# Kernel tuning notes

Hardware: AMD Instinct MI355X
Metric: run time of the kernel (lower is better)

## Reference

```python
import jax, jax.numpy as jnp
from jax import lax
import numpy as np

EPS_COS = 1e-8   # cosine-similarity eps (matches F.cosine_similarity default scale)
EPS_IN = 1e-5    # InstanceNorm2d default eps
NEG = -1e9


def _conv3(x, w, b):
    # x: [B,C,H,W], w: [O,I,3,3]
    y = lax.conv_general_dilated(x, w, (1, 1), 'SAME',
                                 dimension_numbers=('NCHW', 'OIHW', 'NCHW'))
    return y + b[None, :, None, None]


def _inorm(x):
    m = jnp.mean(x, axis=(2, 3), keepdims=True)
    v = jnp.var(x, axis=(2, 3), keepdims=True)
    return (x - m) * lax.rsqrt(v + EPS_IN)


def _shift(former, latter, mask):
    # former/latter: [B,C,H,W]; mask: [H,W] int (1 = hole).
    # For every masked pixel, find the most cosine-similar UNMASKED pixel in the
    # latter (known-region encoder) features and copy the former feature from it.
    B, C, H, W = former.shape
    L = H * W
    lat = lax.stop_gradient(latter).reshape(B, C, L)           # attention is non-differentiable
    latn = lat / (jnp.linalg.norm(lat, axis=1, keepdims=True) + EPS_COS)
    sim = jnp.einsum('bcm,bcn->bmn', latn, latn)               # [B,L,L] query m -> key n
    mflat = mask.reshape(L) > 0
    sim = jnp.where(mflat[None, None, :], NEG, sim)            # keys must be unmasked
    idx = jnp.argmax(sim, axis=-1)                             # [B,L]
    fflat = former.reshape(B, C, L)
    gathered = jnp.take_along_axis(fflat, jnp.broadcast_to(idx[:, None, :], (B, C, L)), axis=2)
    shift = jnp.where(mflat[None, None, :], gathered, 0.0)     # zeros outside the hole
    return shift.reshape(B, C, H, W)


def setup_inputs() -> dict:
    key = jax.random.key(0)
    ks = jax.random.split(key, 6)
    B, C, H, W = 8, 256, 64, 64
    inp = jax.random.normal(ks[0], (B, 2 * C, H, W), dtype=jnp.float32)
    mask = jax.random.randint(ks[1], (H, W), 0, 2, dtype=jnp.int32)
    s1 = 1.0 / float(np.sqrt(2 * C * 9))
    s2 = 1.0 / float(np.sqrt(C * 9))
    W1 = jax.random.uniform(ks[2], (C, 2 * C, 3, 3), jnp.float32, -s1, s1)
    b1 = jax.random.uniform(ks[3], (C,), jnp.float32, -s1, s1)
    W2 = jax.random.uniform(ks[4], (C, C, 3, 3), jnp.float32, -s2, s2)
    b2 = jax.random.uniform(ks[5], (C,), jnp.float32, -s2, s2)
    return {"input": inp, "mask": mask, "W1": W1, "b1": b1, "W2": W2, "b2": b2}


def reference(input, mask, W1, b1, W2, b2):
    C = input.shape[1] // 2
    F_c = input[:, :C]          # former (decoder) features
    F_s = input[:, C:]          # latter (encoder) features
    F_shift = _shift(F_c, F_s, mask)
    F_fuse = F_c * F_shift
    F_com = jnp.concatenate([F_c, F_fuse], axis=1)             # [B,2C,H,W]
    h = jax.nn.relu(_inorm(_conv3(F_com, W1, b1)))
    res = _inorm(_conv3(h, W2, b2))
    return jnp.concatenate([F_c + res, F_s], axis=1)
```

## Files before the change

kernel.cpp:

```cpp
#include <hip/hip_runtime.h>
#include <hip/hip_bf16.h>
#include <math.h>

#define L 4096
#define C 256
#define B 8

typedef __attribute__((ext_vector_type(8))) short bf16x8;
typedef __attribute__((ext_vector_type(8))) ushort u16x8;
typedef __attribute__((ext_vector_type(4))) float f32x4;

__device__ inline ushort f2bu(float f) { __hip_bfloat16 h = __float2bfloat16(f); return *(ushort*)&h; }
__device__ inline float bu2f(ushort u) { __hip_bfloat16 h; *(ushort*)&h = u; return __bfloat162float(h); }

#define SWZ(c) ((((c) >> 1) & 3) << 4)

__global__ __launch_bounds__(256) void compact_mask(
    const int* __restrict__ mask, int* __restrict__ counts,
    int* __restrict__ maskedOrig, int* __restrict__ unmaskOrig,
    int* __restrict__ posOf)
{
    __shared__ int smM[256], smU[256];
    int t = threadIdx.x;
    int flags[16];
    int cm = 0, cu = 0;
    for (int k = 0; k < 16; ++k) {
        int l = t * 16 + k;
        int f = mask[l] > 0;
        flags[k] = f;
        cm += f; cu += !f;
    }
    smM[t] = cm; smU[t] = cu;
    __syncthreads();
    for (int off = 1; off < 256; off <<= 1) {
        int vM = 0, vU = 0;
        if (t >= off) { vM = smM[t - off]; vU = smU[t - off]; }
        __syncthreads();
        smM[t] += vM; smU[t] += vU;
        __syncthreads();
    }
    if (t == 255) { counts[0] = smM[255]; counts[1] = smU[255]; }
    int pm = smM[t] - cm, pu = smU[t] - cu;
    for (int k = 0; k < 16; ++k) {
        int l = t * 16 + k;
        if (flags[k]) { maskedOrig[pm] = l; posOf[l] = pm; pm++; }
        else          { unmaskOrig[pu] = l; posOf[l] = pu; pu++; }
    }
}

__global__ __launch_bounds__(256) void norm_transpose(
    const float* __restrict__ input, const int* __restrict__ mask,
    const int* __restrict__ counts, const int* __restrict__ posOf,
    ushort* __restrict__ fsnh, ushort* __restrict__ fsnl)
{
    int bx = blockIdx.x;
    int b = bx >> 7;
    int l0 = (bx & 127) * 32;
    __shared__ float tile[256 * 33];
    __shared__ float part[8 * 33];
    __shared__ float denom[32];
    __shared__ int   rowdst[32];
    int t = threadIdx.x;
    int lsub = t & 31, cg = t >> 5;
    for (int cc = 0; cc < 256; cc += 8) {
        int c = cc + cg;
        tile[c * 33 + lsub] = input[((size_t)(b * 512 + 256 + c)) * L + l0 + lsub];
    }
    __syncthreads();
    float s = 0.f;
    for (int c = cg; c < 256; c += 8) { float v = tile[c * 33 + lsub]; s = fmaf(v, v, s); }
    part[cg * 33 + lsub] = s;
    __syncthreads();
    if (t < 32) {
        float s2 = 0.f;
        for (int g = 0; g < 8; ++g) s2 += part[g * 33 + t];
        denom[t] = sqrtf(s2) + 1e-8f;
        int l = l0 + t;
        int Nm = counts[0];
        rowdst[t] = (mask[l] > 0) ? posOf[l] : (Nm + posOf[l]);
    }
    __syncthreads();
    for (int ls = 0; ls < 32; ++ls) {
        int r = rowdst[ls];
        float d = denom[ls];
        float val = tile[t * 33 + ls] / d;
        ushort h = f2bu(val);
        float hf = bu2f(h);
        ushort lo = f2bu(val - hf);
        size_t o = ((size_t)b * L + r) * C + t;
        fsnh[o] = h;
        fsnl[o] = lo;
    }
}

__global__ __launch_bounds__(256, 2) void sim_argmax_v6(
    const ushort* __restrict__ hi, const ushort* __restrict__ lo,
    const int* __restrict__ counts,
    float* __restrict__ pval, int* __restrict__ pidx)
{
    __shared__ ushort ldsB[2 * 64 * 256];
    const int Nm = counts[0], Nu = counts[1];
    const int b = blockIdx.z;
    const int m0 = blockIdx.y * 64;
    const int half = blockIdx.x;
    const int t = threadIdx.x;
    const int w = t >> 6, l = t & 63;
    const int lm = l & 15, lk = l >> 4;
    const int key = lm << 4;

    const int nct = (Nu + 63) >> 6;
    const int hs = (nct + 1) >> 1;
    const int cA = half * hs, cB = half ? nct : hs;

    float bestv[4]; int bestn[4];
#pragma unroll
    for (int r = 0; r < 4; ++r) { bestv[r] = -3e38f; bestn[r] = 0; }

    if (m0 < Nm && cA < cB) {
        const char* bytesH = (const char*)hi;
        const char* bytesL = (const char*)lo;
        const size_t bL = (size_t)b * L;
        char* ldsc = (char*)ldsB;

#define STAGE(cc) do { \
    size_t gb = (bL + (size_t)Nm + (size_t)(cc) * 64) * 512; \
    _Pragma("unroll") \
    for (int i = 0; i < 8; ++i) { \
        int j = w * 8 + i; \
        int x = j * 1024 + l * 16; \
        int sx = x ^ (((x >> 9) & 15) << 4); \
        __builtin_amdgcn_global_load_lds((const __attribute__((address_space(1))) unsigned*)(bytesH + gb + sx), \
            (__attribute__((address_space(3))) unsigned*)(ldsc + j * 1024), 16, 0, 0); \
        __builtin_amdgcn_global_load_lds((const __attribute__((address_space(1))) unsigned*)(bytesL + gb + sx), \
            (__attribute__((address_space(3))) unsigned*)(ldsc + 32768 + j * 1024), 16, 0, 0); \
    } \
} while (0)

        STAGE(cA);

        const int rA = m0 + w * 16 + lm;
        bf16x8 ah[8], al[8];
        {
            const ushort* aH = hi + (bL + rA) * C + lk * 8;
            const ushort* aL = lo + (bL + rA) * C + lk * 8;
#pragma unroll
            for (int ks = 0; ks < 8; ++ks) {
                ah[ks] = *(const bf16x8*)(aH + ks * 32);
                al[ks] = *(const bf16x8*)(aL + ks * 32);
            }
        }

        for (int c = cA; c < cB; ++c) {
            asm volatile("s_waitcnt vmcnt(0)" ::: "memory");
            __syncthreads();
            f32x4 acc[4];
#pragma unroll
            for (int nf = 0; nf < 4; ++nf) acc[nf] = (f32x4){0.f, 0.f, 0.f, 0.f};
#pragma unroll
            for (int ks = 0; ks < 8; ++ks) {
                bf16x8 bh[4], bl[4];
#pragma unroll
                for (int nf = 0; nf < 4; ++nf) {
                    int row = nf * 16 + lm;
                    int addr = row * 512 + ((ks * 64 + lk * 16) ^ key);
                    bh[nf] = *(const bf16x8*)(ldsc + addr);
                    bl[nf] = *(const bf16x8*)(ldsc + 32768 + addr);
                }
#pragma unroll
                for (int nf = 0; nf < 4; ++nf)
                    acc[nf] = __builtin_amdgcn_mfma_f32_16x16x32_bf16(ah[ks], bh[nf], acc[nf], 0, 0, 0);
#pragma unroll
                for (int nf = 0; nf < 4; ++nf)
                    acc[nf] = __builtin_amdgcn_mfma_f32_16x16x32_bf16(ah[ks], bl[nf], acc[nf], 0, 0, 0);
#pragma unroll
                for (int nf = 0; nf < 4; ++nf)
                    acc[nf] = __builtin_amdgcn_mfma_f32_16x16x32_bf16(al[ks], bh[nf], acc[nf], 0, 0, 0);
            }
            __syncthreads();
            if (c + 1 < cB) STAGE(c + 1);
            int nbase = c * 64;
#pragma unroll
            for (int r = 0; r < 4; ++r) {
#pragma unroll
                for (int nf = 0; nf < 4; ++nf) {
                    int n = nbase + nf * 16 + lm;
                    float v = acc[nf][r];
                    if (n < Nu && v > bestv[r]) { bestv[r] = v; bestn[r] = n; }
                }
            }
        }
#undef STAGE
    }

    if (m0 >= Nm) return;
#pragma unroll
    for (int r = 0; r < 4; ++r) {
        float bv = bestv[r]; int bn = bestn[r];
#pragma unroll
        for (int mk = 1; mk < 16; mk <<= 1) {
            float ov = __shfl_xor(bv, mk, 64);
            int   on = __shfl_xor(bn, mk, 64);
            if (ov > bv || (ov == bv && on < bn)) { bv = ov; bn = on; }
        }
        if (lm == 0) {
            int m = m0 + w * 16 + lk * 4 + r;
            size_t o = ((size_t)(b * 4096 + m)) * 2 + half;
            pval[o] = bv; pidx[o] = bn;
        }
    }
}

__global__ __launch_bounds__(256) void wprep(
    const float* __restrict__ W1, const float* __restrict__ W2,
    ushort* __restrict__ W1bf, ushort* __restrict__ W2bf)
{
    int gid = blockIdx.x * 256 + threadIdx.x;
    const int N1 = 256 * 512 * 9;
    const int N2 = 256 * 256 * 9;
    if (gid < N1) {
        int ci = gid & 511; int rest = gid >> 9;
        int tau = rest % 9; int co = rest / 9;
        W1bf[gid] = f2bu(W1[((size_t)(co * 512 + ci)) * 9 + tau]);
    } else if (gid < N1 + N2) {
        int g = gid - N1;
        int ci = g & 255; int rest = g >> 8;
        int tau = rest % 9; int co = rest / 9;
        W2bf[g] = f2bu(W2[((size_t)(co * 256 + ci)) * 9 + tau]);
    }
}

__global__ __launch_bounds__(256) void in_prep1(
    const float* __restrict__ input, ushort* __restrict__ inT)
{
    int b = blockIdx.y;
    int p0 = blockIdx.x * 32;
    __shared__ float tile[256][33];
    int t = threadIdx.x;
    int pq = t & 7;
    for (int cc = 0; cc < 256; cc += 32) {
        int ci = cc + (t >> 3);
        float4 v = *(const float4*)(input + ((size_t)(b * 512 + ci)) * L + p0 + pq * 4);
        tile[ci][pq * 4 + 0] = v.x; tile[ci][pq * 4 + 1] = v.y;
        tile[ci][pq * 4 + 2] = v.z; tile[ci][pq * 4 + 3] = v.w;
    }
    __syncthreads();
    int c8 = t & 31;
    for (int pp = 0; pp < 32; pp += 8) {
        int pixloc = pp + (t >> 5);
        u16x8 u;
#pragma unroll
        for (int j = 0; j < 8; ++j) u[j] = f2bu(tile[c8 * 8 + j][pixloc]);
        *(u16x8*)(inT + ((size_t)(b * 4096 + p0 + pixloc)) * 512 + c8 * 8) = u;
    }
}

__global__ __launch_bounds__(256) void in_prep2(
    ushort* __restrict__ inT, const int* __restrict__ mask,
    const float* __restrict__ pval, const int* __restrict__ pidx,
    const int* __restrict__ posOf, const int* __restrict__ unmaskOrig)
{
    int gid = blockIdx.x * 256 + threadIdx.x;
    int c8 = gid & 31;
    int pix = (gid >> 5) & 4095;
    int b = gid >> 17;
    u16x8 out8;
    if (mask[pix] > 0) {
        int m = posOf[pix];
        size_t base = ((size_t)(b * 4096 + m)) * 2;
        float bv = pval[base]; int bn = pidx[base];
        float v1 = pval[base + 1]; int n1 = pidx[base + 1];
        if (v1 > bv || (v1 == bv && n1 < bn)) { bn = n1; }
        int n = unmaskOrig[bn];
        const ushort* rp = inT + ((size_t)(b * 4096 + pix)) * 512 + c8 * 8;
        const ushort* rn = inT + ((size_t)(b * 4096 + n)) * 512 + c8 * 8;
        u16x8 a = *(const u16x8*)rp;
        u16x8 bb = *(const u16x8*)rn;
#pragma unroll
        for (int j = 0; j < 8; ++j) out8[j] = f2bu(bu2f(a[j]) * bu2f(bb[j]));
    } else {
#pragma unroll
        for (int j = 0; j < 8; ++j) out8[j] = 0;
    }
    *(u16x8*)(inT + ((size_t)(b * 4096 + pix)) * 512 + 256 + c8 * 8) = out8;
}

template<int CKROW, int NORM_IN>
__global__ __launch_bounds__(256, 2) void conv_mfma(
    const ushort* __restrict__ Abf, const ushort* __restrict__ Wbf,
    const float* __restrict__ mrsIn,
    ushort* __restrict__ outH, float* __restrict__ psum)
{
    __shared__ float4 ldsv[62208 / 16];
    char* lds = (char*)ldsv;
    char* ldsB = lds + 25344;
    const int t = threadIdx.x;
    const int w = t >> 6;
    const int l = t & 63;
    const int lm = l & 15, lk = l >> 4;
    const int b = blockIdx.z;
    const int y0 = blockIdx.x * 4;
    const int c0 = blockIdx.y * 64;
    const int yw = y0 + w;
    const size_t abase = (size_t)b * 4096 * CKROW;

    f32x4 acc[4][4];
#pragma unroll
    for (int g = 0; g < 4; ++g)
#pragma unroll
        for (int nf = 0; nf < 4; ++nf) acc[g][nf] = (f32x4){0.f, 0.f, 0.f, 0.f};

    if (t < 48) {
        int r = t >> 3;
        int hX = ((t >> 2) & 1) ? 65 : 0;
        int hk = t & 3;
        *(float4*)(lds + (r * 66 + hX) * 64 + ((hk * 16) ^ SWZ(hX))) = (float4){0.f,0.f,0.f,0.f};
    }

    const int NKC = CKROW / 32;
    for (int kc = 0; kc < NKC; ++kc) {
        __syncthreads();
        {
            int x = t >> 2;
            int k8 = t & 3;
            int cX = x + 1;
            char* dbase = lds + cX * 64 + ((k8 * 16) ^ SWZ(cX));
            if (NORM_IN) {
                const float* mb = mrsIn + (size_t)b * 512 + (size_t)(kc * 32 + k8 * 8) * 2;
                float mm[8], rr[8];
#pragma unroll
                for (int j = 0; j < 8; ++j) { mm[j] = mb[2 * j]; rr[j] = mb[2 * j + 1]; }
#pragma unroll
                for (int r = 0; r < 6; ++r) {
                    int yy = y0 - 1 + r;
                    float4 ov = (float4){0.f, 0.f, 0.f, 0.f};
                    if (yy >= 0 && yy < 64) {
                        float4 v = *(const float4*)(Abf + abase + (size_t)(yy * 64 + x) * CKROW + kc * 32 + k8 * 8);
                        u16x8 u = *(u16x8*)&v;
                        u16x8 o;
#pragma unroll
                        for (int j = 0; j < 8; ++j) {
                            float z = (bu2f(u[j]) - mm[j]) * rr[j];
                            o[j] = f2bu(z > 0.f ? z : 0.f);
                        }
                        ov = *(float4*)&o;
                    }
                    *(float4*)(dbase + r * (66 * 64)) = ov;
                }
            } else {
#pragma unroll
                for (int r = 0; r < 6; ++r) {
                    int yy = y0 - 1 + r;
                    float4 v;
                    if (yy >= 0 && yy < 64)
                        v = *(const float4*)(Abf + abase + (size_t)(yy * 64 + x) * CKROW + kc * 32 + k8 * 8);
                    else
                        v = (float4){0.f, 0.f, 0.f, 0.f};
                    *(float4*)(dbase + r * (66 * 64)) = v;
                }
            }
            int cl = t >> 2;
            char* dbaseB = ldsB + cl * 64 + ((k8 * 16) ^ SWZ(cl));
            const ushort* sbase = Wbf + ((size_t)(c0 + cl) * 9) * CKROW + kc * 32 + k8 * 8;
#pragma unroll
            for (int tau = 0; tau < 9; ++tau) {
                *(float4*)(dbaseB + tau * (64 * 64)) = *(const float4*)(sbase + (size_t)tau * CKROW);
            }
        }
        __syncthreads();
#pragma unroll
        for (int ky = 0; ky < 3; ++ky) {
            int r = w + ky;
#pragma unroll
            for (int kx = 0; kx < 3; ++kx) {
                int tau = ky * 3 + kx;
                bf16x8 bfr[4];
#pragma unroll
                for (int nf = 0; nf < 4; ++nf) {
                    int cl = nf * 16 + lm;
                    bfr[nf] = *(bf16x8*)(ldsB + (tau * 64 + cl) * 64 + ((lk * 16) ^ SWZ(cl)));
                }
#pragma unroll
                for (int g = 0; g < 4; ++g) {
                    int aX = g * 16 + lm + kx;
                    bf16x8 afr = *(bf16x8*)(lds + (r * 66 + aX) * 64 + ((lk * 16) ^ SWZ(aX)));
#pragma unroll
                    for (int nf = 0; nf < 4; ++nf)
                        acc[g][nf] = __builtin_amdgcn_mfma_f32_16x16x32_bf16(afr, bfr[nf], acc[g][nf], 0, 0, 0);
                }
            }
        }
    }

#pragma unroll
    for (int g = 0; g < 4; ++g)
#pragma unroll
        for (int nf = 0; nf < 4; ++nf) {
            int cout = c0 + nf * 16 + lm;
#pragma unroll
            for (int r = 0; r < 4; ++r) {
                int pix = yw * 64 + g * 16 + lk * 4 + r;
                outH[((size_t)(b * 4096 + pix)) * 256 + cout] = f2bu(acc[g][nf][r]);
            }
        }

    float s[4], q[4];
#pragma unroll
    for (int nf = 0; nf < 4; ++nf) {
        float ss = 0.f, qq = 0.f;
#pragma unroll
        for (int g = 0; g < 4; ++g)
#pragma unroll
            for (int r = 0; r < 4; ++r) { float v = acc[g][nf][r]; ss += v; qq = fmaf(v, v, qq); }
        ss += __shfl_xor(ss, 16, 64); ss += __shfl_xor(ss, 32, 64);
        qq += __shfl_xor(qq, 16, 64); qq += __shfl_xor(qq, 32, 64);
        s[nf] = ss; q[nf] = qq;
    }
    __syncthreads();
    float* S = (float*)lds;
    float* Q = (float*)(lds + 1024);
    if (l < 16) {
#pragma unroll
        for (int nf = 0; nf < 4; ++nf) {
            S[w * 64 + nf * 16 + l] = s[nf];
            Q[w * 64 + nf * 16 + l] = q[nf];
        }
    }
    __syncthreads();
    if (t < 64) {
        float ts = 0.f, tq = 0.f;
#pragma unroll
        for (int w2 = 0; w2 < 4; ++w2) { ts += S[w2 * 64 + t]; tq += Q[w2 * 64 + t]; }
        size_t o = (((size_t)(b * 256 + c0 + t)) * 16 + blockIdx.x) * 2;
        psum[o] = ts; psum[o + 1] = tq;
    }
}

__global__ __launch_bounds__(256) void stats_reduce(
    const float* __restrict__ psum, float* __restrict__ mrs)
{
    int b = blockIdx.x;
    int c = threadIdx.x;
    float s = 0.f, q = 0.f;
    size_t base = ((size_t)(b * 256 + c)) * 16;
    for (int k = 0; k < 16; ++k) { s += psum[(base + k) * 2]; q += psum[(base + k) * 2 + 1]; }
    float mean = s * (1.f / 4096.f);
    float var = q * (1.f / 4096.f) - mean * mean;
    float rs = rsqrtf(var + 1e-5f);
    mrs[(b * 256 + c) * 2] = mean;
    mrs[(b * 256 + c) * 2 + 1] = rs;
}

__global__ __launch_bounds__(256) void finalize_fs(
    const ushort* __restrict__ resbf, const float* __restrict__ mrs,
    const float* __restrict__ input, float* __restrict__ out)
{
    __shared__ float tileT[256][33];
    int bx = blockIdx.x;
    int t = threadIdx.x;
    if (bx < 8192) {
        size_t i = (size_t)bx * 256 + t;
        size_t b = i >> 18;
        size_t r = i & 262143;
        size_t o = ((size_t)(b * 512 + 256)) * 1024 + r;
        ((float4*)out)[o] = ((const float4*)input)[o];
        return;
    }
    int fb = bx - 8192;
    int b = fb >> 7;
    int p0 = (fb & 127) * 32;
    int c8 = t & 31;
    for (int pp = 0; pp < 32; pp += 8) {
        int pixloc = pp + (t >> 5);
        u16x8 u = *(const u16x8*)(resbf + (((size_t)(b * 4096 + p0 + pixloc)) << 8) + c8 * 8);
#pragma unroll
        for (int j = 0; j < 8; ++j) tileT[c8 * 8 + j][pixloc] = bu2f(u[j]);
    }
    __syncthreads();
    int pq = t & 7;
    for (int cc = 0; cc < 256; cc += 32) {
        int c = cc + (t >> 3);
        float m = mrs[(b * 256 + c) * 2];
        float rs = mrs[(b * 256 + c) * 2 + 1];
        size_t off = ((size_t)(b * 512 + c)) * L + p0 + pq * 4;
        float4 f = *(const float4*)(input + off);
        float4 o;
        o.x = f.x + (tileT[c][pq * 4 + 0] - m) * rs;
        o.y = f.y + (tileT[c][pq * 4 + 1] - m) * rs;
        o.z = f.z + (tileT[c][pq * 4 + 2] - m) * rs;
        o.w = f.w + (tileT[c][pq * 4 + 3] - m) * rs;
        *(float4*)(out + off) = o;
    }
}

extern "C" void kernel_launch(void* const* d_in, const int* in_sizes, int n_in,
                              void* d_out, int out_size, void* d_ws, size_t ws_size,
                              hipStream_t stream) {
    const float* input = (const float*)d_in[0];
    const int*   mask  = (const int*)d_in[1];
    const float* W1    = (const float*)d_in[2];
    const float* W2    = (const float*)d_in[4];
    float* out = (float*)d_out;
    (void)in_sizes; (void)n_in; (void)out_size; (void)ws_size;

    char* ob = (char*)d_out;
    char* wp = (char*)d_ws;

    ushort* fsnh = (ushort*)ob;
    ushort* fsnl = (ushort*)(ob + 16777216);
    float*  pval = (float*)(ob + 33554432);
    int*    pidx = (int*)(ob + 37748736);
    ushort* inT  = (ushort*)ob;
    ushort* hraw = (ushort*)(ob + 33554432);

    ushort* resbf  = (ushort*)wp;
    ushort* W1bf   = (ushort*)(wp + 16777216);
    ushort* W2bf   = (ushort*)(wp + 19136512);
    float*  psum1  = (float*)(wp + 20316160);
    float*  psum2  = (float*)(wp + 20578304);
    float*  mrs1   = (float*)(wp + 20840448);
    float*  mrs2   = (float*)(wp + 20856832);
    int* counts     = (int*)(wp + 20873216);
    int* maskedOrig = counts + 4;
    int* unmaskOrig = maskedOrig + L;
    int* posOf      = unmaskOrig + L;

    compact_mask<<<1, 256, 0, stream>>>(mask, counts, maskedOrig, unmaskOrig, posOf);
    norm_transpose<<<1024, 256, 0, stream>>>(input, mask, counts, posOf, fsnh, fsnl);
    sim_argmax_v6<<<dim3(2, 64, 8), 256, 0, stream>>>(fsnh, fsnl, counts, pval, pidx);
    wprep<<<6912, 256, 0, stream>>>(W1, W2, W1bf, W2bf);
    in_prep1<<<dim3(128, 8), 256, 0, stream>>>(input, inT);
    in_prep2<<<4096, 256, 0, stream>>>(inT, mask, pval, pidx, posOf, unmaskOrig);
    conv_mfma<512, 0><<<dim3(16, 4, 8), 256, 0, stream>>>(inT, W1bf, (const float*)nullptr, hraw, psum1);
    stats_reduce<<<8, 256, 0, stream>>>(psum1, mrs1);
    conv_mfma<256, 1><<<dim3(16, 4, 8), 256, 0, stream>>>(hraw, W2bf, mrs1, resbf, psum2);
    stats_reduce<<<8, 256, 0, stream>>>(psum2, mrs2);
    finalize_fs<<<9216, 256, 0, stream>>>(resbf, mrs2, input, out);
}
```

Baseline: 266.9 us.

## Double-buffer key tiles in sim_argmax with 32-key chunks and async prefetch

The similarity/argmax kernel now stages 32-key chunks into two LDS buffers and prefetches chunk c+2 while computing chunk c. It waits only on the older loads (vmcnt(8)) and uses plain s_barrier instead of a full drain. This is meant to overlap global-to-LDS loads with the MFMA work, which were serialized before. In exchange each chunk does half the MFMAs per barrier, so per-iteration sync and argmax overhead doubles relative to compute.

Result: no change. 270.3 us (+1.3%).

```diff
diff --git a/kernel.cpp b/kernel.cpp
--- a/kernel.cpp
+++ b/kernel.cpp
@@ -93,12 +93,12 @@
     }
 }
 
-__global__ __launch_bounds__(256, 2) void sim_argmax_v6(
+__global__ __launch_bounds__(256, 2) void sim_argmax_v8(
     const ushort* __restrict__ hi, const ushort* __restrict__ lo,
     const int* __restrict__ counts,
     float* __restrict__ pval, int* __restrict__ pidx)
 {
-    __shared__ ushort ldsB[2 * 64 * 256];
+    __shared__ ushort ldsB[32768];
     const int Nm = counts[0], Nu = counts[1];
     const int b = blockIdx.z;
     const int m0 = blockIdx.y * 64;
@@ -108,7 +108,7 @@
     const int lm = l & 15, lk = l >> 4;
     const int key = lm << 4;
 
-    const int nct = (Nu + 63) >> 6;
+    const int nct = (Nu + 31) >> 5;
     const int hs = (nct + 1) >> 1;
     const int cA = half * hs, cB = half ? nct : hs;
 
@@ -122,21 +122,21 @@
         const size_t bL = (size_t)b * L;
         char* ldsc = (char*)ldsB;
 
-#define STAGE(cc) do { \
-    size_t gb = (bL + (size_t)Nm + (size_t)(cc) * 64) * 512; \
+#define STAGE(bofs, cc) do { \
+    size_t gb = (bL + (size_t)Nm + (size_t)(cc) * 32) * 512; \
     _Pragma("unroll") \
-    for (int i = 0; i < 8; ++i) { \
-        int j = w * 8 + i; \
-        int x = j * 1024 + l * 16; \
+    for (int i = 0; i < 4; ++i) { \
+        int x = i * 4096 + t * 16; \
         int sx = x ^ (((x >> 9) & 15) << 4); \
         __builtin_amdgcn_global_load_lds((const __attribute__((address_space(1))) unsigned*)(bytesH + gb + sx), \
-            (__attribute__((address_space(3))) unsigned*)(ldsc + j * 1024), 16, 0, 0); \
+            (__attribute__((address_space(3))) unsigned*)(ldsc + (bofs) + x), 16, 0, 0); \
         __builtin_amdgcn_global_load_lds((const __attribute__((address_space(1))) unsigned*)(bytesL + gb + sx), \
-            (__attribute__((address_space(3))) unsigned*)(ldsc + 32768 + j * 1024), 16, 0, 0); \
+            (__attribute__((address_space(3))) unsigned*)(ldsc + (bofs) + 16384 + x), 16, 0, 0); \
     } \
 } while (0)
 
-        STAGE(cA);
+        STAGE(0, cA);
+        if (cA + 1 < cB) STAGE(32768, cA + 1);
 
         const int rA = m0 + w * 16 + lm;
         bf16x8 ah[8], al[8];
@@ -151,38 +151,40 @@
         }
 
         for (int c = cA; c < cB; ++c) {
-            asm volatile("s_waitcnt vmcnt(0)" ::: "memory");
-            __syncthreads();
-            f32x4 acc[4];
-#pragma unroll
-            for (int nf = 0; nf < 4; ++nf) acc[nf] = (f32x4){0.f, 0.f, 0.f, 0.f};
+            int bob = ((c - cA) & 1) * 32768;
+            if (c + 1 < cB) asm volatile("s_waitcnt vmcnt(8)" ::: "memory");
+            else            asm volatile("s_waitcnt vmcnt(0)" ::: "memory");
+            __builtin_amdgcn_s_barrier();
+            const char* cbase = ldsc + bob;
+            f32x4 acc[2];
+            acc[0] = (f32x4){0.f, 0.f, 0.f, 0.f};
+            acc[1] = (f32x4){0.f, 0.f, 0.f, 0.f};
 #pragma unroll
             for (int ks = 0; ks < 8; ++ks) {
-                bf16x8 bh[4], bl[4];
-#pragma unroll
-                for (int nf = 0; nf < 4; ++nf) {
-                    int row = nf * 16 + lm;
-                    int addr = row * 512 + ((ks * 64 + lk * 16) ^ key);
-                    bh[nf] = *(const bf16x8*)(ldsc + addr);
-                    bl[nf] = *(const bf16x8*)(ldsc + 32768 + addr);
+                bf16x8 bh[2], bl[2];
+#pragma unroll
+                for (int nf = 0; nf < 2; ++nf) {
+                    int addr = (nf * 16 + lm) * 512 + ((ks * 64 + lk * 16) ^ key);
+                    bh[nf] = *(const bf16x8*)(cbase + addr);
+                    bl[nf] = *(const bf16x8*)(cbase + 16384 + addr);
                 }
 #pragma unroll
-                for (int nf = 0; nf < 4; ++nf)
+                for (int nf = 0; nf < 2; ++nf)
                     acc[nf] = __builtin_amdgcn_mfma_f32_16x16x32_bf16(ah[ks], bh[nf], acc[nf], 0, 0, 0);
 #pragma unroll
-                for (int nf = 0; nf < 4; ++nf)
+                for (int nf = 0; nf < 2; ++nf)
                     acc[nf] = __builtin_amdgcn_mfma_f32_16x16x32_bf16(ah[ks], bl[nf], acc[nf], 0, 0, 0);
 #pragma unroll
-                for (int nf = 0; nf < 4; ++nf)
+                for (int nf = 0; nf < 2; ++nf)
                     acc[nf] = __builtin_amdgcn_mfma_f32_16x16x32_bf16(al[ks], bh[nf], acc[nf], 0, 0, 0);
             }
-            __syncthreads();
-            if (c + 1 < cB) STAGE(c + 1);
-            int nbase = c * 64;
+            __builtin_amdgcn_s_barrier();
+            if (c + 2 < cB) STAGE(bob, c + 2);
+            int nbase = c * 32;
 #pragma unroll
             for (int r = 0; r < 4; ++r) {
 #pragma unroll
-                for (int nf = 0; nf < 4; ++nf) {
+                for (int nf = 0; nf < 2; ++nf) {
                     int n = nbase + nf * 16 + lm;
                     float v = acc[nf][r];
                     if (n < Nu && v > bestv[r]) { bestv[r] = v; bestn[r] = n; }
@@ -526,7 +528,7 @@
 
     compact_mask<<<1, 256, 0, stream>>>(mask, counts, maskedOrig, unmaskOrig, posOf);
     norm_transpose<<<1024, 256, 0, stream>>>(input, mask, counts, posOf, fsnh, fsnl);
-    sim_argmax_v6<<<dim3(2, 64, 8), 256, 0, stream>>>(fsnh, fsnl, counts, pval, pidx);
+    sim_argmax_v8<<<dim3(2, 64, 8), 256, 0, stream>>>(fsnh, fsnl, counts, pval, pidx);
     wprep<<<6912, 256, 0, stream>>>(W1, W2, W1bf, W2bf);
     in_prep1<<<dim3(128, 8), 256, 0, stream>>>(input, inT);
     in_prep2<<<4096, 256, 0, stream>>>(inT, mask, pval, pidx, posOf, unmaskOrig);
```
